# Kernel tuning notes

Measured on AMD Instinct MI355X. Metric: run time of the kernel, lower is better.

Reference implementation:

```python
import jax, jax.numpy as jnp
import numpy as np
from jax import lax

N, R, W, H = 256, 32, 8, 6       # batch, n_rooms, room width/height
MX, MY = 72, 72                  # map grid
EMB = 6                          # room embedding width
CIN = 10 + EMB                   # conv input channels


def _boundaries(m):
    # m: [R, W, H] binary room masks -> [R, 4, W, H] (left, right, up, down edges)
    left = jnp.concatenate([m[:, :1, :], jnp.clip(m[:, 1:, :] - m[:, :-1, :], 0)], axis=1)
    right = jnp.concatenate([jnp.clip(m[:, :-1, :] - m[:, 1:, :], 0), m[:, -1:, :]], axis=1)
    up = jnp.concatenate([m[:, :, :1], jnp.clip(m[:, :, 1:] - m[:, :, :-1], 0)], axis=2)
    down = jnp.concatenate([jnp.clip(m[:, :, :-1] - m[:, :, 1:], 0), m[:, :, -1:]], axis=2)
    return jnp.stack([left, right, up, down], axis=1)


def setup_inputs() -> dict:
    key = jax.random.key(0)
    ks = jax.random.split(key, 12)
    room_map = (jax.random.uniform(ks[0], (R, W, H)) < 0.7).astype(jnp.float32)
    room_map = room_map.at[:, 0, 0].set(1.0)  # guarantee nonempty rooms
    doors = (jax.random.uniform(ks[1], (R, 4, W, H)) < 0.15).astype(jnp.float32) * room_map[:, None]
    room_tensor = jnp.concatenate([room_map[:, None], doors, _boundaries(room_map)], axis=1)  # [R,9,W,H]
    px = jax.random.randint(ks[2], (N, R), 0, MX - W)
    py = jax.random.randint(ks[3], (N, R), 0, MY - H)
    room_positions = jnp.stack([px, py], axis=-1).astype(jnp.int32)  # [N,R,2]

    def rn(k, shape, fan_in):
        return jax.random.normal(k, shape, jnp.float32) / np.float32(np.sqrt(fan_in))

    inp = dict(room_positions=room_positions, room_tensor=room_tensor)
    inp['room_embedding'] = jax.random.normal(ks[4], (R, EMB), jnp.float32)
    inp['w_conv1'] = rn(ks[5], (64, CIN, 5, 5), CIN * 25); inp['b_conv1'] = jnp.zeros((64,), jnp.float32)
    inp['w_conv2'] = rn(ks[6], (64, 64, 3, 3), 64 * 9);    inp['b_conv2'] = jnp.zeros((64,), jnp.float32)
    inp['w_conv3'] = rn(ks[7], (64, 64, 3, 3), 64 * 9);    inp['b_conv3'] = jnp.zeros((64,), jnp.float32)
    inp['w_room1'] = rn(ks[8], (128, 64), 64);   inp['b_room1'] = jnp.zeros((128,), jnp.float32)
    inp['w_room2'] = rn(ks[9], (128, 128), 128); inp['b_room2'] = jnp.zeros((128,), jnp.float32)
    inp['w_fc1'] = rn(ks[10], (256, 128), 128);  inp['b_fc1'] = jnp.zeros((256,), jnp.float32)
    inp['w_fc2'] = rn(ks[11], (256, 256), 256);  inp['b_fc2'] = jnp.zeros((256,), jnp.float32)
    return inp


def _conv2d_relu(x, w, b):
    pad = w.shape[-1] // 2
    y = lax.conv_general_dilated(x, w, (1, 1), [(pad, pad), (pad, pad)],
                                 dimension_numbers=('NCHW', 'OIHW', 'NCHW'))
    return jax.nn.relu(y + b[None, :, None, None])


def _forward(room_positions, room_tensor, room_embedding,
             w_conv1, b_conv1, w_conv2, b_conv2, w_conv3, b_conv3,
             w_room1, b_room1, w_room2, b_room2, w_fc1, b_fc1, w_fc2, b_fc2):
    room_map = room_tensor[:, 0]                      # [R,W,H]
    px = room_positions[..., 0]                       # [N,R]
    py = room_positions[..., 1]
    # ---- encode_map: scatter-add all rooms into grid ----
    bidx = jnp.arange(N)[:, None, None, None, None]
    cidx = jnp.arange(9)[None, None, :, None, None]
    ix = px[:, :, None, None, None] + jnp.arange(W)[None, None, None, :, None]   # [N,R,1,W,1]
    iy = py[:, :, None, None, None] + jnp.arange(H)[None, None, None, None, :]   # [N,R,1,1,H]
    map9 = jnp.zeros((N, 9, MX, MY), jnp.float32).at[bidx, cidx, ix, iy].add(room_tensor[None])
    eidx = jnp.arange(EMB)[None, None, :, None, None]
    evals = room_embedding[:, :, None, None] * room_map[:, None, :, :]           # [R,EMB,W,H]
    embg = jnp.zeros((N, EMB, MX, MY), jnp.float32).at[bidx, eidx, ix, iy].add(evals[None])
    X = jnp.concatenate([map9, jnp.ones((N, 1, MX, MY), jnp.float32), embg], axis=1)  # [N,16,MX,MY]
    # ---- map convs ----
    X = _conv2d_relu(X, w_conv1, b_conv1)
    X = _conv2d_relu(X, w_conv2, b_conv2)
    X = _conv2d_relu(X, w_conv3, b_conv3)
    # ---- decode_map: gather room tiles, masked mean per room ----
    Xt = jnp.transpose(X, (0, 2, 3, 1))                                          # [N,MX,MY,C]
    g = Xt[jnp.arange(N)[:, None, None, None],
           px[:, :, None, None] + jnp.arange(W)[None, None, :, None],
           py[:, :, None, None] + jnp.arange(H)[None, None, None, :]]            # [N,R,W,H,C]
    g = g * room_map[None, :, :, :, None]
    room_feat = g.sum(axis=(2, 3)) / room_map.sum(axis=(1, 2))[None, :, None]    # [N,R,C]
    X = jnp.transpose(room_feat, (0, 2, 1))                                      # [N,C,R]
    # ---- 1x1 conv1d room layers ----
    X = jax.nn.relu(jnp.einsum('ncr,oc->nor', X, w_room1) + b_room1[None, :, None])
    X = jax.nn.relu(jnp.einsum('ncr,oc->nor', X, w_room2) + b_room2[None, :, None])
    # ---- fc head: sum over rooms, MLP ----
    X = X.sum(axis=2)                                                            # [N,128]
    X = jax.nn.relu(X @ w_fc1.T + b_fc1)
    return X @ w_fc2.T + b_fc2                                                   # [N,256]


def reference(room_positions, room_tensor, room_embedding,
              w_conv1, b_conv1, w_conv2, b_conv2, w_conv3, b_conv3,
              w_room1, b_room1, w_room2, b_room2, w_fc1, b_fc1, w_fc2, b_fc2):
    return _forward(room_positions, room_tensor, room_embedding,
                    w_conv1, b_conv1, w_conv2, b_conv2, w_conv3, b_conv3,
                    w_room1, b_room1, w_room2, b_room2, w_fc1, b_fc1, w_fc2, b_fc2)
```

## Files before the change

### kernel.cpp

```cpp
#include <hip/hip_runtime.h>
#include <hip/hip_bf16.h>
#include <cstddef>

#define NB 256
#define RR 32
#define WW 8
#define HH 6
#define MXY 72
#define EMB 6
#define CIN1 16

typedef __bf16 bf16x8 __attribute__((ext_vector_type(8)));
typedef float floatx4 __attribute__((ext_vector_type(4)));

static const size_t B_W1F  = 0;
static const size_t B_W2F  = 57344;
static const size_t B_W3F  = 131072;
static const size_t B_RAUX = 204800;
static const size_t B_RINV = 205056;
static const size_t B_HEAD = 205312;
static const size_t F_WR1T = 0;
static const size_t F_WR2T = 8192;
static const size_t F_F1T  = 24576;
static const size_t F_F2T  = 57344;
static const size_t B_FEAT = 696832;
static const size_t B_IMSK = 2793984;

__device__ inline short f2b(float f) {
    unsigned u = __builtin_bit_cast(unsigned, f);
    unsigned r = (u + 0x7fffu + ((u >> 16) & 1u)) >> 16;
    return (short)r;
}

__global__ void prep_all(const float* __restrict__ w1, const float* __restrict__ w2,
                         const float* __restrict__ w3, const float* __restrict__ wr1,
                         const float* __restrict__ wr2, const float* __restrict__ wf1,
                         const float* __restrict__ wf2, const float* __restrict__ rt,
                         const int* __restrict__ pos, char* __restrict__ ws)
{
    short* W1F = (short*)(ws + B_W1F);
    short* W2F = (short*)(ws + B_W2F);
    short* W3F = (short*)(ws + B_W3F);
    float* HEAD = (float*)(ws + B_HEAD);

    int idx = blockIdx.x * 256 + threadIdx.x;
    if (idx < 28672) {
        int j = idx & 7, lane = (idx >> 3) & 63, nt = (idx >> 9) & 3, kk = idx >> 11;
        int k = kk * 32 + (lane >> 4) * 8 + j;
        int oc = nt * 16 + (lane & 15);
        int tap = k >> 4, ci = k & 15;
        float v = (tap < 25) ? w1[(oc * 16 + ci) * 25 + tap] : 0.f;
        W1F[idx] = f2b(v);
        return;
    }
    idx -= 28672;
    if (idx < 36864) {
        int j = idx & 7, lane = (idx >> 3) & 63, nt = (idx >> 9) & 3, kk = idx >> 11;
        int k = kk * 32 + (lane >> 4) * 8 + j;
        int oc = nt * 16 + (lane & 15);
        int tap = k >> 6, cp = k & 63;
        int ci = (cp >> 2) + (cp & 3) * 16;
        W2F[idx] = f2b(w2[(oc * 64 + ci) * 9 + tap]);
        return;
    }
    idx -= 36864;
    if (idx < 36864) {
        int j = idx & 7, lane = (idx >> 3) & 63, nt = (idx >> 9) & 3, kk = idx >> 11;
        int k = kk * 32 + (lane >> 4) * 8 + j;
        int oc = nt * 16 + (lane & 15);
        int tap = k >> 6, cp = k & 63;
        int ci = (cp >> 2) + (cp & 3) * 16;
        W3F[idx] = f2b(w3[(oc * 64 + ci) * 9 + tap]);
        return;
    }
    idx -= 36864;
    if (idx < 8192)  { int o = idx & 127, c = idx >> 7; HEAD[F_WR1T + idx] = wr1[o * 64 + c]; return; }
    idx -= 8192;
    if (idx < 16384) { int o = idx & 127, c = idx >> 7; HEAD[F_WR2T + idx] = wr2[o * 128 + c]; return; }
    idx -= 16384;
    if (idx < 32768) { int o = idx & 255, c = idx >> 8; HEAD[F_F1T + idx] = wf1[o * 128 + c]; return; }
    idx -= 32768;
    if (idx < 65536) { int o = idx & 255, c = idx >> 8; HEAD[F_F2T + idx] = wf2[o * 256 + c]; return; }
    idx -= 65536;
    if (idx < 8192) {
        const int n = idx >> 5, r0 = idx & 31;
        const int px0 = pos[(n * RR + r0) * 2 + 0];
        const int py0 = pos[(n * RR + r0) * 2 + 1];
        unsigned m = 0;
        for (int r = 0; r < RR; ++r) {
            int rpx = pos[(n * RR + r) * 2 + 0];
            int rpy = pos[(n * RR + r) * 2 + 1];
            if (rpx >= px0 - 11 && rpx <= px0 + 11 && rpy >= py0 - 9 && rpy <= py0 + 9)
                m |= 1u << r;
        }
        ((unsigned*)(ws + B_IMSK))[n * RR + r0] = m;
        return;
    }
    idx -= 8192;
    if (idx < RR) {
        unsigned long long m = 0ull;
        int cnt = 0;
        for (int j = 0; j < WW * HH; ++j)
            if (rt[idx * 9 * 48 + j] != 0.f) { m |= (1ull << j); ++cnt; }
        ((unsigned long long*)(ws + B_RAUX))[idx] = m;
        ((float*)(ws + B_RINV))[idx] = 1.f / (float)cnt;
    }
}

__global__ __launch_bounds__(256, 5) void fused_conv(
    const unsigned* __restrict__ imask, const float* __restrict__ rt,
    const float* __restrict__ emb, const short* __restrict__ wAll,
    const float* __restrict__ bc1, const float* __restrict__ bc2,
    const float* __restrict__ bc3, const int* __restrict__ pos,
    const unsigned long long* __restrict__ rmask, float* __restrict__ feat)
{
    __shared__ __align__(16) short s_Y1[120 * 72];
    __shared__ __align__(16) short s_u[80 * 72];
    __shared__ float s_feat[64];

    const int tid = threadIdx.x;
    const int lane = tid & 63;
    const int wv = tid >> 6;
    const int ml = lane & 15;
    const int q = lane >> 4;
    const int room = blockIdx.x;
    const int n = blockIdx.y;

    const int px = pos[(n * RR + room) * 2 + 0];
    const int py = pos[(n * RR + room) * 2 + 1];

    const short* W1F = wAll;
    const short* W2F = wAll + B_W2F / 2;
    const short* W3F = wAll + B_W3F / 2;

    bf16x8 Bb[2][4];
    auto load_k = [&](const short* wF, int kk, bf16x8* dst) {
        const short* src = wF + (size_t)kk * 2048;
#pragma unroll
        for (int j2 = 0; j2 < 4; ++j2)
            dst[j2] = *reinterpret_cast<const bf16x8*>(src + (j2 * 64 + lane) * 8);
    };

    load_k(W1F, 0, Bb[0]);

    {
        const unsigned mk0 = imask[n * RR + room];
        if (tid < 224) {
            const int row = tid / 14, col = tid - (tid / 14) * 14;
            const int gx = px - 4 + row, gy = py - 4 + col;
            float a[16];
#pragma unroll
            for (int c = 0; c < 16; ++c) a[c] = 0.f;
            a[9] = ((unsigned)gx < (unsigned)MXY && (unsigned)gy < (unsigned)MXY) ? 1.f : 0.f;

            unsigned mm = mk0;
            while (mm) {
                const int r = __builtin_ctz(mm);
                mm &= mm - 1;
                const int rpx = pos[(n * RR + r) * 2 + 0];
                const int rpy = pos[(n * RR + r) * 2 + 1];
                const int w = gx - rpx, h = gy - rpy;
                if ((unsigned)w < (unsigned)WW && (unsigned)h < (unsigned)HH) {
                    const int j = w * HH + h;
                    const float* rr = rt + r * 9 * 48;
#pragma unroll
                    for (int c = 0; c < 9; ++c) a[c] += rr[c * 48 + j];
                    const float mv = rr[j];
#pragma unroll
                    for (int e = 0; e < EMB; ++e) a[10 + e] += emb[r * EMB + e] * mv;
                }
            }
            short o[16];
#pragma unroll
            for (int c = 0; c < 16; ++c) o[c] = f2b(a[c]);
            *reinterpret_cast<uint4*>(&s_u[tid * 24 + 0]) = *reinterpret_cast<uint4*>(o);
            *reinterpret_cast<uint4*>(&s_u[tid * 24 + 8]) = *reinterpret_cast<uint4*>(o + 8);
        }
    }
    __syncthreads();

    {
        int prow[2], pcol[2];
#pragma unroll
        for (int i = 0; i < 2; ++i) {
            int p = wv * 32 + i * 16 + ml;
            if (p > 119) p = 119;
            prow[i] = p / 10; pcol[i] = p - prow[i] * 10;
        }
        floatx4 acc1[2][4] = {};

#pragma unroll
        for (int kk = 0; kk < 13; ++kk) {
            if (kk < 12) load_k(W1F, kk + 1, Bb[(kk + 1) & 1]);
            else         load_k(W2F, 0, Bb[1]);
            int tap = kk * 2 + (q >> 1);
            if (tap > 24) tap = 24;
            int chb = (q & 1) * 8;
            int dx = tap / 5, dy = tap - dx * 5;
            __builtin_amdgcn_s_setprio(1);
#pragma unroll
            for (int i = 0; i < 2; ++i) {
                bf16x8 A = *reinterpret_cast<const bf16x8*>(
                    &s_u[((prow[i] + dx) * 14 + (pcol[i] + dy)) * 24 + chb]);
#pragma unroll
                for (int j2 = 0; j2 < 4; ++j2)
                    acc1[i][j2] = __builtin_amdgcn_mfma_f32_16x16x32_bf16(
                        A, Bb[kk & 1][j2], acc1[i][j2], 0, 0, 0);
            }
            __builtin_amdgcn_s_setprio(0);
        }
        float b4[4];
#pragma unroll
        for (int j2 = 0; j2 < 4; ++j2) b4[j2] = bc1[j2 * 16 + ml];
#pragma unroll
        for (int i = 0; i < 2; ++i)
#pragma unroll
            for (int r = 0; r < 4; ++r) {
                int p = wv * 32 + i * 16 + q * 4 + r;
                if (p < 120) {
                    unsigned lo = (unsigned)(unsigned short)f2b(fmaxf(acc1[i][0][r] + b4[0], 0.f))
                                | ((unsigned)(unsigned short)f2b(fmaxf(acc1[i][1][r] + b4[1], 0.f)) << 16);
                    unsigned hi = (unsigned)(unsigned short)f2b(fmaxf(acc1[i][2][r] + b4[2], 0.f))
                                | ((unsigned)(unsigned short)f2b(fmaxf(acc1[i][3][r] + b4[3], 0.f)) << 16);
                    *reinterpret_cast<uint2*>(&s_Y1[p * 72 + ml * 4]) = make_uint2(lo, hi);
                }
            }
    }
    __syncthreads();

    {
        int prowA, pcolA, prowB, pcolB;
        {
            int p0 = wv * 16 + ml; prowA = p0 >> 3; pcolA = p0 & 7;
            int p1 = 64 + ml;      prowB = p1 >> 3; pcolB = p1 & 7;
        }
        floatx4 acc2[4] = {};
        floatx4 acc2s = {};

#pragma unroll
        for (int kk = 0; kk < 18; ++kk) {
            if (kk < 17) load_k(W2F, kk + 1, Bb[kk & 1]);
            else         load_k(W3F, 0, Bb[1]);
            bf16x8 B4 = *reinterpret_cast<const bf16x8*>(
                W2F + (size_t)kk * 2048 + (wv * 64 + lane) * 8);
            const int tap = kk >> 1;
            const int chb = (kk & 1) * 32 + q * 8;
            const int dx = tap / 3, dy = tap - (tap / 3) * 3;
            bf16x8 A0 = *reinterpret_cast<const bf16x8*>(
                &s_Y1[((prowA + dx) * 10 + (pcolA + dy)) * 72 + chb]);
            bf16x8 A4 = *reinterpret_cast<const bf16x8*>(
                &s_Y1[((prowB + dx) * 10 + (pcolB + dy)) * 72 + chb]);
            __builtin_amdgcn_s_setprio(1);
#pragma unroll
            for (int j2 = 0; j2 < 4; ++j2)
                acc2[j2] = __builtin_amdgcn_mfma_f32_16x16x32_bf16(A0, Bb[(kk + 1) & 1][j2], acc2[j2], 0, 0, 0);
            acc2s = __builtin_amdgcn_mfma_f32_16x16x32_bf16(A4, B4, acc2s, 0, 0, 0);
            __builtin_amdgcn_s_setprio(0);
        }
        float b4[4];
#pragma unroll
        for (int j2 = 0; j2 < 4; ++j2) b4[j2] = bc2[j2 * 16 + ml];
#pragma unroll
        for (int r = 0; r < 4; ++r) {
            int p = wv * 16 + q * 4 + r;
            unsigned lo = (unsigned)(unsigned short)f2b(fmaxf(acc2[0][r] + b4[0], 0.f))
                        | ((unsigned)(unsigned short)f2b(fmaxf(acc2[1][r] + b4[1], 0.f)) << 16);
            unsigned hi = (unsigned)(unsigned short)f2b(fmaxf(acc2[2][r] + b4[2], 0.f))
                        | ((unsigned)(unsigned short)f2b(fmaxf(acc2[3][r] + b4[3], 0.f)) << 16);
            *reinterpret_cast<uint2*>(&s_u[p * 72 + ml * 4]) = make_uint2(lo, hi);
        }
        {
            float bt = bc2[wv * 16 + ml];
#pragma unroll
            for (int r = 0; r < 4; ++r) {
                int p = 64 + q * 4 + r;
                s_u[p * 72 + ml * 4 + wv] = f2b(fmaxf(acc2s[r] + bt, 0.f));
            }
        }
        if (tid < 64) s_feat[tid] = 0.f;
    }
    __syncthreads();

    if (wv < 3) {
        int p0 = wv * 16 + ml;
        int row3 = p0 / 6, col3 = p0 - (p0 / 6) * 6;
        floatx4 acc3[4] = {};

#pragma unroll
        for (int kk = 0; kk < 18; ++kk) {
            if (kk < 17) load_k(W3F, kk + 1, Bb[kk & 1]);
            const int tap = kk >> 1;
            const int chb = (kk & 1) * 32 + q * 8;
            const int dx = tap / 3, dy = tap - (tap / 3) * 3;
            bf16x8 A = *reinterpret_cast<const bf16x8*>(
                &s_u[((row3 + dx) * 8 + (col3 + dy)) * 72 + chb]);
            __builtin_amdgcn_s_setprio(1);
#pragma unroll
            for (int j2 = 0; j2 < 4; ++j2)
                acc3[j2] = __builtin_amdgcn_mfma_f32_16x16x32_bf16(A, Bb[(kk + 1) & 1][j2], acc3[j2], 0, 0, 0);
            __builtin_amdgcn_s_setprio(0);
        }
        float b4[4];
#pragma unroll
        for (int j2 = 0; j2 < 4; ++j2) b4[j2] = bc3[j2 * 16 + ml];
        float part[4] = {0.f, 0.f, 0.f, 0.f};
        const unsigned long long mk = rmask[room];
#pragma unroll
        for (int r = 0; r < 4; ++r) {
            int p = wv * 16 + q * 4 + r;
            if ((mk >> p) & 1ull) {
#pragma unroll
                for (int j2 = 0; j2 < 4; ++j2)
                    part[j2] += fmaxf(acc3[j2][r] + b4[j2], 0.f);
            }
        }
#pragma unroll
        for (int j2 = 0; j2 < 4; ++j2) {
            part[j2] += __shfl_xor(part[j2], 16);
            part[j2] += __shfl_xor(part[j2], 32);
        }
        if (q == 0) {
#pragma unroll
            for (int j2 = 0; j2 < 4; ++j2)
                atomicAdd(&s_feat[j2 * 16 + ml], part[j2]);
        }
    }
    __syncthreads();
    if (tid < 64)
        feat[((size_t)n * RR + room) * 64 + tid] = s_feat[tid];
}

__global__ __launch_bounds__(256) void mlp_head(const float* __restrict__ feat,
                                                const float* __restrict__ HEAD,
                                                const float* __restrict__ rinv,
                                                const float* __restrict__ b1,
                                                const float* __restrict__ b2,
                                                const float* __restrict__ bf1,
                                                const float* __restrict__ bf2,
                                                float* __restrict__ outp)
{
    __shared__ __align__(16) float s_feat[RR * 64];
    __shared__ __align__(16) float s_h1[RR * 128];
    __shared__ __align__(16) float s_s[2 * 128];
    __shared__ __align__(16) float s_sf[128];
    __shared__ __align__(16) float s_t1[256];

    const int n = blockIdx.x;
    const int tid = threadIdx.x;
    const float* W1t = HEAD + F_WR1T;
    const float* W2t = HEAD + F_WR2T;
    const float* F1t = HEAD + F_F1T;
    const float* F2t = HEAD + F_F2T;

    for (int i = tid; i < RR * 64; i += 256)
        s_feat[i] = feat[(size_t)n * RR * 64 + i] * rinv[i >> 6];
    __syncthreads();

    const int o = tid & 127;
    const int rh = tid >> 7;

    float acc[16];
#pragma unroll
    for (int r = 0; r < 16; ++r) acc[r] = b1[o];
    for (int c4 = 0; c4 < 16; ++c4) {
        float w0 = W1t[(c4 * 4 + 0) * 128 + o];
        float w1 = W1t[(c4 * 4 + 1) * 128 + o];
        float w2 = W1t[(c4 * 4 + 2) * 128 + o];
        float w3 = W1t[(c4 * 4 + 3) * 128 + o];
#pragma unroll
        for (int r = 0; r < 16; ++r) {
            float4 f = *reinterpret_cast<const float4*>(&s_feat[(rh * 16 + r) * 64 + c4 * 4]);
            acc[r] += f.x * w0 + f.y * w1 + f.z * w2 + f.w * w3;
        }
    }
#pragma unroll
    for (int r = 0; r < 16; ++r) s_h1[(rh * 16 + r) * 128 + o] = fmaxf(acc[r], 0.f);
    __syncthreads();

#pragma unroll
    for (int r = 0; r < 16; ++r) acc[r] = b2[o];
    for (int c4 = 0; c4 < 32; ++c4) {
        float w0 = W2t[(c4 * 4 + 0) * 128 + o];
        float w1 = W2t[(c4 * 4 + 1) * 128 + o];
        float w2 = W2t[(c4 * 4 + 2) * 128 + o];
        float w3 = W2t[(c4 * 4 + 3) * 128 + o];
#pragma unroll
        for (int r = 0; r < 16; ++r) {
            float4 f = *reinterpret_cast<const float4*>(&s_h1[(rh * 16 + r) * 128 + c4 * 4]);
            acc[r] += f.x * w0 + f.y * w1 + f.z * w2 + f.w * w3;
        }
    }
    float ps = 0.f;
#pragma unroll
    for (int r = 0; r < 16; ++r) ps += fmaxf(acc[r], 0.f);
    s_s[rh * 128 + o] = ps;
    __syncthreads();
    if (tid < 128) s_sf[tid] = s_s[tid] + s_s[128 + tid];
    __syncthreads();

    {
        float a = bf1[tid];
        for (int c4 = 0; c4 < 32; ++c4) {
            float4 f = *reinterpret_cast<const float4*>(&s_sf[c4 * 4]);
            a += f.x * F1t[(c4 * 4 + 0) * 256 + tid];
            a += f.y * F1t[(c4 * 4 + 1) * 256 + tid];
            a += f.z * F1t[(c4 * 4 + 2) * 256 + tid];
            a += f.w * F1t[(c4 * 4 + 3) * 256 + tid];
        }
        s_t1[tid] = fmaxf(a, 0.f);
    }
    __syncthreads();

    {
        float a = bf2[tid];
        for (int c4 = 0; c4 < 64; ++c4) {
            float4 f = *reinterpret_cast<const float4*>(&s_t1[c4 * 4]);
            a += f.x * F2t[(c4 * 4 + 0) * 256 + tid];
            a += f.y * F2t[(c4 * 4 + 1) * 256 + tid];
            a += f.z * F2t[(c4 * 4 + 2) * 256 + tid];
            a += f.w * F2t[(c4 * 4 + 3) * 256 + tid];
        }
        outp[(size_t)n * 256 + tid] = a;
    }
}

extern "C" void kernel_launch(void* const* d_in, const int* in_sizes, int n_in,
                              void* d_out, int out_size, void* d_ws, size_t ws_size,
                              hipStream_t stream)
{
    const int* pos = (const int*)d_in[0];
    const float* rt = (const float*)d_in[1];
    const float* emb = (const float*)d_in[2];
    const float* w1 = (const float*)d_in[3];
    const float* bc1 = (const float*)d_in[4];
    const float* w2 = (const float*)d_in[5];
    const float* bc2 = (const float*)d_in[6];
    const float* w3 = (const float*)d_in[7];
    const float* bc3 = (const float*)d_in[8];
    const float* wr1 = (const float*)d_in[9];
    const float* br1 = (const float*)d_in[10];
    const float* wr2 = (const float*)d_in[11];
    const float* br2 = (const float*)d_in[12];
    const float* wf1 = (const float*)d_in[13];
    const float* bf1 = (const float*)d_in[14];
    const float* wf2 = (const float*)d_in[15];
    const float* bf2 = (const float*)d_in[16];
    float* out = (float*)d_out;
    char* ws = (char*)d_ws;

    prep_all<<<913, 256, 0, stream>>>(w1, w2, w3, wr1, wr2, wf1, wf2, rt, pos, ws);

    const short* WALL = (const short*)(ws + B_W1F);
    const unsigned long long* RMASK = (const unsigned long long*)(ws + B_RAUX);
    const float* RINV = (const float*)(ws + B_RINV);
    float* HEAD = (float*)(ws + B_HEAD);
    float* FEAT = (float*)(ws + B_FEAT);
    unsigned* IMSK = (unsigned*)(ws + B_IMSK);

    fused_conv<<<dim3(RR, NB), 256, 0, stream>>>(IMSK, rt, emb, WALL,
                                                 bc1, bc2, bc3, pos, RMASK, FEAT);

    mlp_head<<<NB, 256, 0, stream>>>(FEAT, HEAD, RINV, br1, br2, bf1, bf2, out);
}
```

Measured before the change: 313.9 us.

## Split MLP head into per-room-quarter and FC kernels; relax conv launch bounds

The MLP head is split in two. The room-layer part runs over 4 room quarters per sample (1024 blocks instead of 256), and each block atomically adds its partial room sum into a zeroed workspace buffer. A separate kernel then runs the fc1/fc2 layers from that buffer. prep_all gains extra blocks to zero the buffer, and fused_conv's minimum-blocks hint drops from 5 to 4, which allows more registers per thread at the cost of possible lower occupancy. The split adds one kernel launch and float atomics, so the summation order becomes nondeterministic.

```diff
diff --git a/kernel.cpp b/kernel.cpp
--- a/kernel.cpp
+++ b/kernel.cpp
@@ -25,6 +25,7 @@
 static const size_t F_F2T  = 57344;
 static const size_t B_FEAT = 696832;
 static const size_t B_IMSK = 2793984;
+static const size_t B_SSUM = 2826752;
 
 __device__ inline short f2b(float f) {
     unsigned u = __builtin_bit_cast(unsigned, f);
@@ -104,10 +105,13 @@
             if (rt[idx * 9 * 48 + j] != 0.f) { m |= (1ull << j); ++cnt; }
         ((unsigned long long*)(ws + B_RAUX))[idx] = m;
         ((float*)(ws + B_RINV))[idx] = 1.f / (float)cnt;
-    }
-}
-
-__global__ __launch_bounds__(256, 5) void fused_conv(
+        return;
+    }
+    idx -= RR;
+    if (idx < NB * 128) ((float*)(ws + B_SSUM))[idx] = 0.f;
+}
+
+__global__ __launch_bounds__(256, 4) void fused_conv(
     const unsigned* __restrict__ imask, const float* __restrict__ rt,
     const float* __restrict__ emb, const short* __restrict__ wAll,
     const float* __restrict__ bc1, const float* __restrict__ bc2,
@@ -330,76 +334,90 @@
         feat[((size_t)n * RR + room) * 64 + tid] = s_feat[tid];
 }
 
-__global__ __launch_bounds__(256) void mlp_head(const float* __restrict__ feat,
-                                                const float* __restrict__ HEAD,
-                                                const float* __restrict__ rinv,
-                                                const float* __restrict__ b1,
-                                                const float* __restrict__ b2,
-                                                const float* __restrict__ bf1,
-                                                const float* __restrict__ bf2,
-                                                float* __restrict__ outp)
+__global__ __launch_bounds__(256) void head_rooms(const float* __restrict__ feat,
+                                                  const float* __restrict__ HEAD,
+                                                  const float* __restrict__ rinv,
+                                                  const float* __restrict__ b1,
+                                                  const float* __restrict__ b2,
+                                                  float* __restrict__ ssum)
 {
-    __shared__ __align__(16) float s_feat[RR * 64];
-    __shared__ __align__(16) float s_h1[RR * 128];
+    __shared__ __align__(16) float s_feat[8 * 64];
+    __shared__ __align__(16) float s_h1[8 * 128];
     __shared__ __align__(16) float s_s[2 * 128];
-    __shared__ __align__(16) float s_sf[128];
-    __shared__ __align__(16) float s_t1[256];
-
-    const int n = blockIdx.x;
+
+    const int qr = blockIdx.x;
+    const int n = blockIdx.y;
     const int tid = threadIdx.x;
     const float* W1t = HEAD + F_WR1T;
     const float* W2t = HEAD + F_WR2T;
-    const float* F1t = HEAD + F_F1T;
-    const float* F2t = HEAD + F_F2T;
-
-    for (int i = tid; i < RR * 64; i += 256)
-        s_feat[i] = feat[(size_t)n * RR * 64 + i] * rinv[i >> 6];
+
+    for (int i = tid; i < 8 * 64; i += 256)
+        s_feat[i] = feat[(size_t)n * RR * 64 + qr * 512 + i] * rinv[qr * 8 + (i >> 6)];
     __syncthreads();
 
     const int o = tid & 127;
     const int rh = tid >> 7;
 
-    float acc[16];
-#pragma unroll
-    for (int r = 0; r < 16; ++r) acc[r] = b1[o];
+    float acc[4];
+#pragma unroll
+    for (int r = 0; r < 4; ++r) acc[r] = b1[o];
     for (int c4 = 0; c4 < 16; ++c4) {
         float w0 = W1t[(c4 * 4 + 0) * 128 + o];
         float w1 = W1t[(c4 * 4 + 1) * 128 + o];
         float w2 = W1t[(c4 * 4 + 2) * 128 + o];
         float w3 = W1t[(c4 * 4 + 3) * 128 + o];
 #pragma unroll
-        for (int r = 0; r < 16; ++r) {
-            float4 f = *reinterpret_cast<const float4*>(&s_feat[(rh * 16 + r) * 64 + c4 * 4]);
+        for (int r = 0; r < 4; ++r) {
+            float4 f = *reinterpret_cast<const float4*>(&s_feat[(rh * 4 + r) * 64 + c4 * 4]);
             acc[r] += f.x * w0 + f.y * w1 + f.z * w2 + f.w * w3;
         }
     }
 #pragma unroll
-    for (int r = 0; r < 16; ++r) s_h1[(rh * 16 + r) * 128 + o] = fmaxf(acc[r], 0.f);
-    __syncthreads();
-
-#pragma unroll
-    for (int r = 0; r < 16; ++r) acc[r] = b2[o];
+    for (int r = 0; r < 4; ++r) s_h1[(rh * 4 + r) * 128 + o] = fmaxf(acc[r], 0.f);
+    __syncthreads();
+
+#pragma unroll
+    for (int r = 0; r < 4; ++r) acc[r] = b2[o];
     for (int c4 = 0; c4 < 32; ++c4) {
         float w0 = W2t[(c4 * 4 + 0) * 128 + o];
         float w1 = W2t[(c4 * 4 + 1) * 128 + o];
         float w2 = W2t[(c4 * 4 + 2) * 128 + o];
         float w3 = W2t[(c4 * 4 + 3) * 128 + o];
 #pragma unroll
-        for (int r = 0; r < 16; ++r) {
-            float4 f = *reinterpret_cast<const float4*>(&s_h1[(rh * 16 + r) * 128 + c4 * 4]);
+        for (int r = 0; r < 4; ++r) {
+            float4 f = *reinterpret_cast<const float4*>(&s_h1[(rh * 4 + r) * 128 + c4 * 4]);
             acc[r] += f.x * w0 + f.y * w1 + f.z * w2 + f.w * w3;
         }
     }
     float ps = 0.f;
 #pragma unroll
-    for (int r = 0; r < 16; ++r) ps += fmaxf(acc[r], 0.f);
+    for (int r = 0; r < 4; ++r) ps += fmaxf(acc[r], 0.f);
     s_s[rh * 128 + o] = ps;
     __syncthreads();
-    if (tid < 128) s_sf[tid] = s_s[tid] + s_s[128 + tid];
+    if (tid < 128)
+        atomicAdd(&ssum[(size_t)n * 128 + tid], s_s[tid] + s_s[128 + tid]);
+}
+
+__global__ __launch_bounds__(256) void head_fc(const float* __restrict__ ssum,
+                                               const float* __restrict__ HEAD,
+                                               const float* __restrict__ bf1,
+                                               const float* __restrict__ bf2,
+                                               float* __restrict__ outp)
+{
+    __shared__ __align__(16) float s_sf[128];
+    __shared__ __align__(16) float s_t1[256];
+
+    const int n = blockIdx.x;
+    const int tid = threadIdx.x;
+    const float* F1t = HEAD + F_F1T;
+    const float* F2t = HEAD + F_F2T;
+
+    if (tid < 128) s_sf[tid] = ssum[(size_t)n * 128 + tid];
     __syncthreads();
 
     {
         float a = bf1[tid];
+#pragma unroll 4
         for (int c4 = 0; c4 < 32; ++c4) {
             float4 f = *reinterpret_cast<const float4*>(&s_sf[c4 * 4]);
             a += f.x * F1t[(c4 * 4 + 0) * 256 + tid];
@@ -413,6 +431,7 @@
 
     {
         float a = bf2[tid];
+#pragma unroll 4
         for (int c4 = 0; c4 < 64; ++c4) {
             float4 f = *reinterpret_cast<const float4*>(&s_t1[c4 * 4]);
             a += f.x * F2t[(c4 * 4 + 0) * 256 + tid];
@@ -448,7 +467,7 @@
     float* out = (float*)d_out;
     char* ws = (char*)d_ws;
 
-    prep_all<<<913, 256, 0, stream>>>(w1, w2, w3, wr1, wr2, wf1, wf2, rt, pos, ws);
+    prep_all<<<1041, 256, 0, stream>>>(w1, w2, w3, wr1, wr2, wf1, wf2, rt, pos, ws);
 
     const short* WALL = (const short*)(ws + B_W1F);
     const unsigned long long* RMASK = (const unsigned long long*)(ws + B_RAUX);
@@ -456,9 +475,11 @@
     float* HEAD = (float*)(ws + B_HEAD);
     float* FEAT = (float*)(ws + B_FEAT);
     unsigned* IMSK = (unsigned*)(ws + B_IMSK);
+    float* SSUM = (float*)(ws + B_SSUM);
 
     fused_conv<<<dim3(RR, NB), 256, 0, stream>>>(IMSK, rt, emb, WALL,
                                                  bc1, bc2, bc3, pos, RMASK, FEAT);
 
-    mlp_head<<<NB, 256, 0, stream>>>(FEAT, HEAD, RINV, br1, br2, bf1, bf2, out);
-}
+    head_rooms<<<dim3(4, NB), 256, 0, stream>>>(FEAT, HEAD, RINV, br1, br2, SSUM);
+    head_fc<<<NB, 256, 0, stream>>>(SSUM, HEAD, bf1, bf2, out);
+}
```

New measurement: 298.9 us. -4.8%, faster.

## Fuse room MLP and head into conv kernel with last-block reduction

Applied to the files above, without the earlier changes.

Removes the separate mlp_head kernel. Each (room, batch) block now computes its own room1/room2 layers and atomically adds the result into a per-batch sum. A counter picks the last block per batch, which then runs the fc head. The prep kernel gains work to zero the sum and counter buffers. This saves a launch and the feature round trip through memory, at the cost of atomics, a threadfence, and launch bounds lowered from 5 to 4 blocks, which may reduce occupancy of the conv part.

```diff
diff --git a/kernel.cpp b/kernel.cpp
--- a/kernel.cpp
+++ b/kernel.cpp
@@ -23,8 +23,9 @@
 static const size_t F_WR2T = 8192;
 static const size_t F_F1T  = 24576;
 static const size_t F_F2T  = 57344;
-static const size_t B_FEAT = 696832;
 static const size_t B_IMSK = 2793984;
+static const size_t B_SSUM = 2826752;
+static const size_t B_CNT  = 2957824;
 
 __device__ inline short f2b(float f) {
     unsigned u = __builtin_bit_cast(unsigned, f);
@@ -104,19 +105,29 @@
             if (rt[idx * 9 * 48 + j] != 0.f) { m |= (1ull << j); ++cnt; }
         ((unsigned long long*)(ws + B_RAUX))[idx] = m;
         ((float*)(ws + B_RINV))[idx] = 1.f / (float)cnt;
-    }
+        return;
+    }
+    idx -= RR;
+    if (idx < NB * 128) { ((float*)(ws + B_SSUM))[idx] = 0.f; return; }
+    idx -= NB * 128;
+    if (idx < NB) ((int*)(ws + B_CNT))[idx] = 0;
 }
 
-__global__ __launch_bounds__(256, 5) void fused_conv(
+__global__ __launch_bounds__(256, 4) void fused_all(
     const unsigned* __restrict__ imask, const float* __restrict__ rt,
     const float* __restrict__ emb, const short* __restrict__ wAll,
     const float* __restrict__ bc1, const float* __restrict__ bc2,
     const float* __restrict__ bc3, const int* __restrict__ pos,
-    const unsigned long long* __restrict__ rmask, float* __restrict__ feat)
+    const unsigned long long* __restrict__ rmask, const float* __restrict__ HEAD,
+    const float* __restrict__ rinv, const float* __restrict__ br1,
+    const float* __restrict__ br2, const float* __restrict__ bf1,
+    const float* __restrict__ bf2, float* __restrict__ ssum,
+    int* __restrict__ cnt, float* __restrict__ outp)
 {
     __shared__ __align__(16) short s_Y1[120 * 72];
     __shared__ __align__(16) short s_u[80 * 72];
     __shared__ float s_feat[64];
+    __shared__ int s_last;
 
     const int tid = threadIdx.x;
     const int lane = tid & 63;
@@ -326,80 +337,70 @@
         }
     }
     __syncthreads();
-    if (tid < 64)
-        feat[((size_t)n * RR + room) * 64 + tid] = s_feat[tid];
-}
-
-__global__ __launch_bounds__(256) void mlp_head(const float* __restrict__ feat,
-                                                const float* __restrict__ HEAD,
-                                                const float* __restrict__ rinv,
-                                                const float* __restrict__ b1,
-                                                const float* __restrict__ b2,
-                                                const float* __restrict__ bf1,
-                                                const float* __restrict__ bf2,
-                                                float* __restrict__ outp)
-{
-    __shared__ __align__(16) float s_feat[RR * 64];
-    __shared__ __align__(16) float s_h1[RR * 128];
-    __shared__ __align__(16) float s_s[2 * 128];
-    __shared__ __align__(16) float s_sf[128];
-    __shared__ __align__(16) float s_t1[256];
-
-    const int n = blockIdx.x;
-    const int tid = threadIdx.x;
-    const float* W1t = HEAD + F_WR1T;
-    const float* W2t = HEAD + F_WR2T;
-    const float* F1t = HEAD + F_F1T;
-    const float* F2t = HEAD + F_F2T;
-
-    for (int i = tid; i < RR * 64; i += 256)
-        s_feat[i] = feat[(size_t)n * RR * 64 + i] * rinv[i >> 6];
+
+    {
+        float* s_ps = (float*)s_u;
+        float* s_h1 = (float*)s_Y1;
+        const int o = tid & 127;
+        const int rh = tid >> 7;
+        const float rv = rinv[room];
+        const float* W1t = HEAD + F_WR1T;
+        const float* W2t = HEAD + F_WR2T;
+
+        float a = 0.f;
+#pragma unroll
+        for (int c4 = 0; c4 < 8; ++c4) {
+            float4 f = *reinterpret_cast<const float4*>(&s_feat[rh * 32 + c4 * 4]);
+            a += f.x * W1t[(rh * 32 + c4 * 4 + 0) * 128 + o];
+            a += f.y * W1t[(rh * 32 + c4 * 4 + 1) * 128 + o];
+            a += f.z * W1t[(rh * 32 + c4 * 4 + 2) * 128 + o];
+            a += f.w * W1t[(rh * 32 + c4 * 4 + 3) * 128 + o];
+        }
+        s_ps[tid] = a;
+        __syncthreads();
+        if (tid < 128)
+            s_h1[tid] = fmaxf(br1[tid] + rv * (s_ps[tid] + s_ps[128 + tid]), 0.f);
+        __syncthreads();
+
+        a = 0.f;
+#pragma unroll
+        for (int c4 = 0; c4 < 16; ++c4) {
+            float4 f = *reinterpret_cast<const float4*>(&s_h1[rh * 64 + c4 * 4]);
+            a += f.x * W2t[(rh * 64 + c4 * 4 + 0) * 128 + o];
+            a += f.y * W2t[(rh * 64 + c4 * 4 + 1) * 128 + o];
+            a += f.z * W2t[(rh * 64 + c4 * 4 + 2) * 128 + o];
+            a += f.w * W2t[(rh * 64 + c4 * 4 + 3) * 128 + o];
+        }
+        s_ps[tid] = a;
+        __syncthreads();
+        if (tid < 128) {
+            float p = fmaxf(br2[tid] + s_ps[tid] + s_ps[128 + tid], 0.f);
+            atomicAdd(&ssum[(size_t)n * 128 + tid], p);
+        }
+    }
+
+    __threadfence();
+    if (tid == 0) {
+        int prev = __hip_atomic_fetch_add(&cnt[n], 1, __ATOMIC_ACQ_REL,
+                                          __HIP_MEMORY_SCOPE_AGENT);
+        s_last = (prev == RR - 1);
+    }
     __syncthreads();
-
-    const int o = tid & 127;
-    const int rh = tid >> 7;
-
-    float acc[16];
-#pragma unroll
-    for (int r = 0; r < 16; ++r) acc[r] = b1[o];
-    for (int c4 = 0; c4 < 16; ++c4) {
-        float w0 = W1t[(c4 * 4 + 0) * 128 + o];
-        float w1 = W1t[(c4 * 4 + 1) * 128 + o];
-        float w2 = W1t[(c4 * 4 + 2) * 128 + o];
-        float w3 = W1t[(c4 * 4 + 3) * 128 + o];
-#pragma unroll
-        for (int r = 0; r < 16; ++r) {
-            float4 f = *reinterpret_cast<const float4*>(&s_feat[(rh * 16 + r) * 64 + c4 * 4]);
-            acc[r] += f.x * w0 + f.y * w1 + f.z * w2 + f.w * w3;
-        }
-    }
-#pragma unroll
-    for (int r = 0; r < 16; ++r) s_h1[(rh * 16 + r) * 128 + o] = fmaxf(acc[r], 0.f);
-    __syncthreads();
-
-#pragma unroll
-    for (int r = 0; r < 16; ++r) acc[r] = b2[o];
-    for (int c4 = 0; c4 < 32; ++c4) {
-        float w0 = W2t[(c4 * 4 + 0) * 128 + o];
-        float w1 = W2t[(c4 * 4 + 1) * 128 + o];
-        float w2 = W2t[(c4 * 4 + 2) * 128 + o];
-        float w3 = W2t[(c4 * 4 + 3) * 128 + o];
-#pragma unroll
-        for (int r = 0; r < 16; ++r) {
-            float4 f = *reinterpret_cast<const float4*>(&s_h1[(rh * 16 + r) * 128 + c4 * 4]);
-            acc[r] += f.x * w0 + f.y * w1 + f.z * w2 + f.w * w3;
-        }
-    }
-    float ps = 0.f;
-#pragma unroll
-    for (int r = 0; r < 16; ++r) ps += fmaxf(acc[r], 0.f);
-    s_s[rh * 128 + o] = ps;
-    __syncthreads();
-    if (tid < 128) s_sf[tid] = s_s[tid] + s_s[128 + tid];
-    __syncthreads();
+    if (!s_last) return;
 
     {
+        float* s_sf = (float*)s_Y1;
+        float* s_t1 = (float*)s_u;
+        const float* F1t = HEAD + F_F1T;
+        const float* F2t = HEAD + F_F2T;
+
+        if (tid < 128)
+            s_sf[tid] = __hip_atomic_load(&ssum[(size_t)n * 128 + tid],
+                                          __ATOMIC_RELAXED, __HIP_MEMORY_SCOPE_AGENT);
+        __syncthreads();
+
         float a = bf1[tid];
+#pragma unroll 4
         for (int c4 = 0; c4 < 32; ++c4) {
             float4 f = *reinterpret_cast<const float4*>(&s_sf[c4 * 4]);
             a += f.x * F1t[(c4 * 4 + 0) * 256 + tid];
@@ -408,11 +409,10 @@
             a += f.w * F1t[(c4 * 4 + 3) * 256 + tid];
         }
         s_t1[tid] = fmaxf(a, 0.f);
-    }
-    __syncthreads();
-
-    {
-        float a = bf2[tid];
+        __syncthreads();
+
+        a = bf2[tid];
+#pragma unroll 4
         for (int c4 = 0; c4 < 64; ++c4) {
             float4 f = *reinterpret_cast<const float4*>(&s_t1[c4 * 4]);
             a += f.x * F2t[(c4 * 4 + 0) * 256 + tid];
@@ -448,17 +448,18 @@
     float* out = (float*)d_out;
     char* ws = (char*)d_ws;
 
-    prep_all<<<913, 256, 0, stream>>>(w1, w2, w3, wr1, wr2, wf1, wf2, rt, pos, ws);
+    prep_all<<<1042, 256, 0, stream>>>(w1, w2, w3, wr1, wr2, wf1, wf2, rt, pos, ws);
 
     const short* WALL = (const short*)(ws + B_W1F);
     const unsigned long long* RMASK = (const unsigned long long*)(ws + B_RAUX);
     const float* RINV = (const float*)(ws + B_RINV);
-    float* HEAD = (float*)(ws + B_HEAD);
-    float* FEAT = (float*)(ws + B_FEAT);
+    const float* HEAD = (const float*)(ws + B_HEAD);
     unsigned* IMSK = (unsigned*)(ws + B_IMSK);
-
-    fused_conv<<<dim3(RR, NB), 256, 0, stream>>>(IMSK, rt, emb, WALL,
-                                                 bc1, bc2, bc3, pos, RMASK, FEAT);
-
-    mlp_head<<<NB, 256, 0, stream>>>(FEAT, HEAD, RINV, br1, br2, bf1, bf2, out);
+    float* SSUM = (float*)(ws + B_SSUM);
+    int* CNT = (int*)(ws + B_CNT);
+
+    fused_all<<<dim3(RR, NB), 256, 0, stream>>>(IMSK, rt, emb, WALL,
+                                                bc1, bc2, bc3, pos, RMASK, HEAD,
+                                                RINV, br1, br2, bf1, bf2,
+                                                SSUM, CNT, out);
 }
```

New measurement: 881.0 us. +180.7%, slower.
